# Kernel optimization log

Hardware: AMD Instinct MI355X
Metric: run time of the kernel (lower is better)

The kernel has to match this reference:

```python
import jax, jax.numpy as jnp
import numpy as np

N_NODES = 200000
N_EDGES = 3200000
NX = 8
NK = 2


def _l2norm(x, eps=1e-12):
    # F.normalize(x, p=2, dim=-1)
    n = jnp.linalg.norm(x, axis=-1, keepdims=True)
    return x / jnp.maximum(n, eps)


def _aniso_conv(x, src, dst, Kw, n_nodes):
    """For each kernel j: out_j[t] = sum_{e: dst[e]=t} Kw[j,e] * x[src[e]].
    Concatenate over kernels along the feature axis."""
    g = x[src]  # [E, d] gather
    def agg(w):  # w: [E]
        return jax.ops.segment_sum(w[:, None] * g, dst, num_segments=n_nodes)
    out = jax.vmap(agg)(Kw)  # [nk, N, d]
    return jnp.transpose(out, (1, 0, 2)).reshape(n_nodes, -1)  # [N, nk*d]


def setup_inputs() -> dict:
    key = jax.random.key(0)
    ks = jax.random.split(key, 8)
    x = jax.random.normal(ks[0], (N_NODES, NX), dtype=jnp.float32)
    src = jax.random.randint(ks[1], (N_EDGES,), 0, N_NODES, dtype=jnp.int64 if jax.config.jax_enable_x64 else jnp.int32)
    dst = jax.random.randint(ks[2], (N_EDGES,), 0, N_NODES, dtype=src.dtype)
    edge_index = jnp.stack([src, dst], axis=0)
    Kw = jax.random.normal(ks[3], (NK, N_EDGES), dtype=jnp.float32)
    d0, d1 = NX * NK, NX * NK * 2          # 16, 32
    d2 = d1 * NK                            # 64
    hidden, out_ch = 128, 64
    W0 = jax.random.normal(ks[4], (d0, d1), dtype=jnp.float32) / np.sqrt(d0)
    b0 = jnp.zeros((d1,), dtype=jnp.float32)
    W1 = jax.random.normal(ks[5], (d2, hidden), dtype=jnp.float32) / np.sqrt(d2)
    b1 = jnp.zeros((hidden,), dtype=jnp.float32)
    W2 = jax.random.normal(ks[6], (hidden, out_ch), dtype=jnp.float32) / np.sqrt(hidden)
    b2 = jnp.zeros((out_ch,), dtype=jnp.float32)
    return {"x": x, "edge_index": edge_index, "Kw": Kw,
            "W0": W0, "b0": b0, "W1": W1, "b1": b1, "W2": W2, "b2": b2}


def reference(x, edge_index, Kw, W0, b0, W1, b1, W2, b2):
    src, dst = edge_index[0], edge_index[1]
    n = x.shape[0]
    # layer 0: AnisoConv -> single-linear MLP -> L2 normalize
    h = _aniso_conv(x, src, dst, Kw, n)      # [N, 16]
    h = h @ W0 + b0                           # [N, 32]
    h = _l2norm(h)
    # layer 1: AnisoConv -> 2-layer MLP (ReLU between) -> L2 normalize
    h = _aniso_conv(h, src, dst, Kw, n)      # [N, 64]
    h = jax.nn.relu(h @ W1 + b1)             # [N, 128]
    h = h @ W2 + b2                           # [N, 64]
    h = _l2norm(h)
    return h
```

## Files before the change

### kernel.cpp

```cpp
#include <hip/hip_runtime.h>

#define NN 200000
#define NE 3200000
#define NB_SCAN 782
#define NBUCK 196
#define BSHIFT 10
#define BMASK 1023
#define SRCMASK 0x3FFFFu
#define NBLK_A 1024
#define EPB (NE / NBLK_A)
#define NPASS 13
#define EMAX 18
#define NT_MLP1 12500

using bf16x8 = __attribute__((ext_vector_type(8))) short;
using f32x4  = __attribute__((ext_vector_type(4))) float;

__device__ __forceinline__ float bflo(unsigned u) { return __uint_as_float(u << 16); }
__device__ __forceinline__ float bfhi(unsigned u) { return __uint_as_float(u & 0xffff0000u); }
__device__ __forceinline__ unsigned short f2bfu(float f) {
  unsigned u = __float_as_uint(f);
  return (unsigned short)((u + 0x7fffu + ((u >> 16) & 1u)) >> 16);
}
__device__ __forceinline__ unsigned pack2(float a, float b) {
  return (unsigned)f2bfu(a) | ((unsigned)f2bfu(b) << 16);
}

__device__ __forceinline__ void acc_edge(uint2 e, uint4 u, float* g0, float* g1) {
  float k0 = bflo(e.y), k1 = bfhi(e.y);
  float v0 = bflo(u.x), v1 = bfhi(u.x);
  float v2 = bflo(u.y), v3 = bfhi(u.y);
  float v4 = bflo(u.z), v5 = bfhi(u.z);
  float v6 = bflo(u.w), v7 = bfhi(u.w);
  g0[0] += k0 * v0; g0[1] += k0 * v1; g0[2] += k0 * v2; g0[3] += k0 * v3;
  g0[4] += k0 * v4; g0[5] += k0 * v5; g0[6] += k0 * v6; g0[7] += k0 * v7;
  g1[0] += k1 * v0; g1[1] += k1 * v1; g1[2] += k1 * v2; g1[3] += k1 * v3;
  g1[4] += k1 * v4; g1[5] += k1 * v5; g1[6] += k1 * v6; g1[7] += k1 * v7;
}


__global__ __launch_bounds__(256) void bhist_kernel(const int* __restrict__ dst,
                                                    int* __restrict__ bhT) {
  __shared__ int h[NBUCK];
  for (int k = threadIdx.x; k < NBUCK; k += 256) h[k] = 0;
  __syncthreads();
  int base = blockIdx.x * EPB;
  for (int i = threadIdx.x; i < EPB; i += 256)
    atomicAdd(&h[dst[base + i] >> BSHIFT], 1);
  __syncthreads();
  for (int k = threadIdx.x; k < NBUCK; k += 256)
    bhT[k * NBLK_A + blockIdx.x] = h[k];
}

__global__ __launch_bounds__(NBLK_A) void bscan_kernel(int* __restrict__ bhT,
                                                       int* __restrict__ btot) {
  __shared__ int s[NBLK_A];
  int b = blockIdx.x;
  int v = bhT[b * NBLK_A + threadIdx.x];
  s[threadIdx.x] = v;
  __syncthreads();
#pragma unroll
  for (int off = 1; off < NBLK_A; off <<= 1) {
    int t = (threadIdx.x >= off) ? s[threadIdx.x - off] : 0;
    __syncthreads();
    s[threadIdx.x] += t;
    __syncthreads();
  }
  bhT[b * NBLK_A + threadIdx.x] = s[threadIdx.x] - v;
  if (threadIdx.x == NBLK_A - 1) btot[b] = s[NBLK_A - 1];
}

__global__ __launch_bounds__(256) void bbase_kernel(const int* __restrict__ btot,
                                                    int* __restrict__ bbase) {
  __shared__ int s[256];
  int v = (threadIdx.x < NBUCK) ? btot[threadIdx.x] : 0;
  s[threadIdx.x] = v;
  __syncthreads();
#pragma unroll
  for (int off = 1; off < 256; off <<= 1) {
    int t = (threadIdx.x >= off) ? s[threadIdx.x - off] : 0;
    __syncthreads();
    s[threadIdx.x] += t;
    __syncthreads();
  }
  if (threadIdx.x < NBUCK) bbase[threadIdx.x] = s[threadIdx.x] - v;
  if (threadIdx.x == NBUCK - 1) bbase[NBUCK] = s[threadIdx.x];
}

__global__ __launch_bounds__(256) void bplace_kernel(
    const int* __restrict__ src, const int* __restrict__ dst,
    const float* __restrict__ kw, const int* __restrict__ bhT,
    const int* __restrict__ bbase, uint2* __restrict__ bsorted) {
  __shared__ int cur[NBUCK];
  for (int k = threadIdx.x; k < NBUCK; k += 256)
    cur[k] = bbase[k] + bhT[k * NBLK_A + blockIdx.x];
  __syncthreads();
  int base = blockIdx.x * EPB;
  for (int i = threadIdx.x; i < EPB; i += 256) {
    int e = base + i;
    int d = dst[e];
    int p = atomicAdd(&cur[d >> BSHIFT], 1);
    uint2 u;
    u.x = (unsigned)src[e] | ((unsigned)(d & BMASK) << 18);
    u.y = pack2(kw[e], kw[NE + e]);
    bsorted[p] = u;
  }
}


__global__ __launch_bounds__(1024) void nsort_kernel(
    const uint2* __restrict__ bsorted, const int* __restrict__ bbase,
    int* __restrict__ cnt, int* __restrict__ offs, uint2* __restrict__ sedge) {
  __shared__ int h[1024];
  __shared__ int cur[1024];
  int tid = threadIdx.x, b = blockIdx.x;
  h[tid] = 0;
  __syncthreads();
  int r0 = bbase[b], r1 = bbase[b + 1];
  int i0 = r0 + tid;

  uint2 e[EMAX];
#pragma unroll
  for (int j = 0; j < EMAX; ++j) {
    int i = i0 + j * 1024;
    if (i < r1) {
      e[j] = bsorted[i];
      atomicAdd(&h[e[j].x >> 18], 1);
    }
  }
  for (int i = i0 + EMAX * 1024; i < r1; i += 1024)
    atomicAdd(&h[bsorted[i].x >> 18], 1);
  __syncthreads();

  int v = h[tid];
  cur[tid] = v;
  __syncthreads();
  for (int off = 1; off < 1024; off <<= 1) {
    int t = (tid >= off) ? cur[tid - off] : 0;
    __syncthreads();
    cur[tid] += t;
    __syncthreads();
  }
  int excl = r0 + cur[tid] - v;
  int node = b * 1024 + tid;
  if (node < NN) { cnt[node] = v; offs[node] = excl; }
  __syncthreads();
  cur[tid] = excl;
  __syncthreads();

  for (int p = 0; p < NPASS; ++p) {
#pragma unroll
    for (int j = 0; j < EMAX; ++j) {
      int i = i0 + j * 1024;
      if (i < r1) {
        unsigned srcv = e[j].x & SRCMASK;
        if ((int)(srcv >> 14) == p) {
          int pos = atomicAdd(&cur[e[j].x >> 18], 1);
          uint2 w; w.x = srcv; w.y = e[j].y;
          sedge[pos] = w;
        }
      }
    }
    __syncthreads();
  }
  for (int i = i0 + EMAX * 1024; i < r1; i += 1024) {
    uint2 u = bsorted[i];
    int pos = atomicAdd(&cur[u.x >> 18], 1);
    u.x &= SRCMASK;
    sedge[pos] = u;
  }
}


__global__ __launch_bounds__(256) void xcvt_kernel(const float* __restrict__ x,
                                                   unsigned short* __restrict__ xbf) {
  int i = blockIdx.x * 256 + threadIdx.x;
  if (i >= NN) return;
  const float4* xp = reinterpret_cast<const float4*>(x + (size_t)i * 8);
  float4 a = xp[0], b = xp[1];
  uint4 u;
  u.x = pack2(a.x, a.y); u.y = pack2(a.z, a.w);
  u.z = pack2(b.x, b.y); u.w = pack2(b.z, b.w);
  *reinterpret_cast<uint4*>(xbf + (size_t)i * 8) = u;
}


__global__ __launch_bounds__(256) void fused0_kernel(
    const unsigned short* __restrict__ xbf, const int* __restrict__ offs,
    const int* __restrict__ cnt, const uint2* __restrict__ sedge,
    const float* __restrict__ W0, const float* __restrict__ b0,
    unsigned short* __restrict__ h1bf) {
  __shared__ float w0t[32][16];
  __shared__ float b0s[32];
  int tid = threadIdx.x;
  for (int i = tid; i < 16 * 32; i += 256) {
    int k = i >> 5, j = i & 31;
    w0t[j][k] = W0[i];
  }
  if (tid < 32) b0s[tid] = b0[tid];
  __syncthreads();

  int node = blockIdx.x * 256 + tid;
  if (node >= NN) return;

  int start = offs[node];
  int deg = cnt[node];
  float ha[8], hb[8];
#pragma unroll
  for (int k = 0; k < 8; ++k) { ha[k] = 0.f; hb[k] = 0.f; }

  int i = 0;
  for (; i + 4 <= deg; i += 4) {
    uint2 ee[4];
    uint4 uu[4];
#pragma unroll
    for (int j = 0; j < 4; ++j) ee[j] = sedge[start + i + j];
#pragma unroll
    for (int j = 0; j < 4; ++j)
      uu[j] = *reinterpret_cast<const uint4*>(xbf + (size_t)ee[j].x * 8);
#pragma unroll
    for (int j = 0; j < 4; ++j) acc_edge(ee[j], uu[j], ha, hb);
  }
  for (; i < deg; ++i) {
    uint2 e = sedge[start + i];
    uint4 u = *reinterpret_cast<const uint4*>(xbf + (size_t)e.x * 8);
    acc_edge(e, u, ha, hb);
  }

  float o[32];
  float ss = 0.f;
#pragma unroll
  for (int j = 0; j < 32; ++j) {
    float acc = b0s[j];
#pragma unroll
    for (int k = 0; k < 8; ++k) acc += ha[k] * w0t[j][k];
#pragma unroll
    for (int k = 0; k < 8; ++k) acc += hb[k] * w0t[j][8 + k];
    o[j] = acc;
    ss += acc * acc;
  }
  float inv = 1.f / fmaxf(sqrtf(ss), 1e-12f);
  uint4* op = reinterpret_cast<uint4*>(h1bf + (size_t)node * 32);
#pragma unroll
  for (int c = 0; c < 4; ++c) {
    uint4 u;
    u.x = pack2(o[c * 8 + 0] * inv, o[c * 8 + 1] * inv);
    u.y = pack2(o[c * 8 + 2] * inv, o[c * 8 + 3] * inv);
    u.z = pack2(o[c * 8 + 4] * inv, o[c * 8 + 5] * inv);
    u.w = pack2(o[c * 8 + 6] * inv, o[c * 8 + 7] * inv);
    op[c] = u;
  }
}


__global__ __launch_bounds__(256) void gather1_kernel(
    const unsigned short* __restrict__ h1bf, const int* __restrict__ offs,
    const int* __restrict__ cnt, const uint2* __restrict__ sedge,
    unsigned short* __restrict__ gbf) {
  int idx = blockIdx.x * 256 + threadIdx.x;
  int node = idx >> 2, q = idx & 3;
  int start = offs[node];
  int deg = cnt[node];

  float g0[8], g1[8];
#pragma unroll
  for (int k = 0; k < 8; ++k) { g0[k] = 0.f; g1[k] = 0.f; }

  int i = 0;
  for (; i + 8 <= deg; i += 8) {
    uint2 ee[8];
    uint4 uu[8];
#pragma unroll
    for (int j = 0; j < 8; ++j) ee[j] = sedge[start + i + j];
#pragma unroll
    for (int j = 0; j < 8; ++j)
      uu[j] = *reinterpret_cast<const uint4*>(h1bf + (size_t)ee[j].x * 32 + q * 8);
#pragma unroll
    for (int j = 0; j < 8; ++j) acc_edge(ee[j], uu[j], g0, g1);
  }
  for (; i + 4 <= deg; i += 4) {
    uint2 ee[4];
    uint4 uu[4];
#pragma unroll
    for (int j = 0; j < 4; ++j) ee[j] = sedge[start + i + j];
#pragma unroll
    for (int j = 0; j < 4; ++j)
      uu[j] = *reinterpret_cast<const uint4*>(h1bf + (size_t)ee[j].x * 32 + q * 8);
#pragma unroll
    for (int j = 0; j < 4; ++j) acc_edge(ee[j], uu[j], g0, g1);
  }
  for (; i < deg; ++i) {
    uint2 e = sedge[start + i];
    uint4 u = *reinterpret_cast<const uint4*>(h1bf + (size_t)e.x * 32 + q * 8);
    acc_edge(e, u, g0, g1);
  }

  uint4 s0, s1;
  s0.x = pack2(g0[0], g0[1]); s0.y = pack2(g0[2], g0[3]);
  s0.z = pack2(g0[4], g0[5]); s0.w = pack2(g0[6], g0[7]);
  s1.x = pack2(g1[0], g1[1]); s1.y = pack2(g1[2], g1[3]);
  s1.z = pack2(g1[4], g1[5]); s1.w = pack2(g1[6], g1[7]);
  *reinterpret_cast<uint4*>(gbf + (size_t)node * 64 + q * 8) = s0;
  *reinterpret_cast<uint4*>(gbf + (size_t)node * 64 + 32 + q * 8) = s1;
}


__global__ __launch_bounds__(256) void mlp1_kernel(
    const unsigned short* __restrict__ gbf,
    const float* __restrict__ W1, const float* __restrict__ b1,
    const float* __restrict__ W2, const float* __restrict__ b2,
    float* __restrict__ out) {
  __shared__ __align__(16) short hlds[4][16][136];
  int tid = threadIdx.x;
  int wave = tid >> 6, lane = tid & 63;
  int lg = lane >> 4;
  int lr = lane & 15;

  bf16x8 w1f[8][2];
#pragma unroll
  for (int n = 0; n < 8; ++n)
#pragma unroll
    for (int ks = 0; ks < 2; ++ks) {
      bf16x8 f;
#pragma unroll
      for (int i = 0; i < 8; ++i)
        f[i] = (short)f2bfu(W1[(size_t)(ks * 32 + lg * 8 + i) * 128 + n * 16 + lr]);
      w1f[n][ks] = f;
    }
  bf16x8 w2f[4][4];
#pragma unroll
  for (int n2 = 0; n2 < 4; ++n2)
#pragma unroll
    for (int ks = 0; ks < 4; ++ks) {
      bf16x8 f;
#pragma unroll
      for (int i = 0; i < 8; ++i)
        f[i] = (short)f2bfu(W2[(size_t)(ks * 32 + lg * 8 + i) * 64 + n2 * 16 + lr]);
      w2f[n2][ks] = f;
    }
  float b1v[8], b2v[4];
#pragma unroll
  for (int n = 0; n < 8; ++n) b1v[n] = b1[n * 16 + lr];
#pragma unroll
  for (int n2 = 0; n2 < 4; ++n2) b2v[n2] = b2[n2 * 16 + lr];

  for (int tile = blockIdx.x * 4 + wave; tile < NT_MLP1; tile += gridDim.x * 4) {
    int base = tile * 16;
    const bf16x8* grow = reinterpret_cast<const bf16x8*>(gbf + (size_t)(base + lr) * 64);
    bf16x8 a1_0 = grow[lg];
    bf16x8 a1_1 = grow[4 + lg];

#pragma unroll
    for (int n = 0; n < 8; ++n) {
      f32x4 acc = {0.f, 0.f, 0.f, 0.f};
      acc = __builtin_amdgcn_mfma_f32_16x16x32_bf16(a1_0, w1f[n][0], acc, 0, 0, 0);
      acc = __builtin_amdgcn_mfma_f32_16x16x32_bf16(a1_1, w1f[n][1], acc, 0, 0, 0);
#pragma unroll
      for (int q = 0; q < 4; ++q) {
        float v = fmaxf(acc[q] + b1v[n], 0.f);
        hlds[wave][lg * 4 + q][n * 16 + lr] = (short)f2bfu(v);
      }
    }

    bf16x8 a2[4];
#pragma unroll
    for (int ks = 0; ks < 4; ++ks)
      a2[ks] = *reinterpret_cast<const bf16x8*>(&hlds[wave][lr][ks * 32 + lg * 8]);
    f32x4 acc2[4];
#pragma unroll
    for (int n2 = 0; n2 < 4; ++n2) {
      f32x4 a = {0.f, 0.f, 0.f, 0.f};
#pragma unroll
      for (int ks = 0; ks < 4; ++ks)
        a = __builtin_amdgcn_mfma_f32_16x16x32_bf16(a2[ks], w2f[n2][ks], a, 0, 0, 0);
      acc2[n2] = a;
    }

#pragma unroll
    for (int q = 0; q < 4; ++q) {
      float s = 0.f;
#pragma unroll
      for (int n2 = 0; n2 < 4; ++n2) {
        float v = acc2[n2][q] + b2v[n2];
        s += v * v;
      }
      s += __shfl_xor(s, 1); s += __shfl_xor(s, 2);
      s += __shfl_xor(s, 4); s += __shfl_xor(s, 8);
      float inv = 1.f / fmaxf(sqrtf(s), 1e-12f);
      size_t rowoff = (size_t)(base + lg * 4 + q) * 64 + lr;
#pragma unroll
      for (int n2 = 0; n2 < 4; ++n2)
        out[rowoff + n2 * 16] = (acc2[n2][q] + b2v[n2]) * inv;
    }
  }
}


extern "C" void kernel_launch(void* const* d_in, const int* in_sizes, int n_in,
                              void* d_out, int out_size, void* d_ws, size_t ws_size,
                              hipStream_t stream) {
  const float* x  = (const float*)d_in[0];
  const int* ei   = (const int*)d_in[1];
  const float* kw = (const float*)d_in[2];
  const float* W0 = (const float*)d_in[3];
  const float* b0 = (const float*)d_in[4];
  const float* W1 = (const float*)d_in[5];
  const float* b1 = (const float*)d_in[6];
  const float* W2 = (const float*)d_in[7];
  const float* b2 = (const float*)d_in[8];
  float* out = (float*)d_out;

  const int* src = ei;
  const int* dst = ei + NE;

  char* p = (char*)d_ws;
  uint2* bsorted = (uint2*)p;                p += (size_t)NE * 8;
  uint2* sedge   = (uint2*)p;                p += (size_t)NE * 8;
  unsigned short* h1bf = (unsigned short*)p; p += (size_t)NN * 32 * 2;
  unsigned short* xbf  = (unsigned short*)p; p += (size_t)NN * 8 * 2;
  int* bhT   = (int*)p;                      p += (size_t)NBUCK * NBLK_A * 4;
  int* btot  = (int*)p;                      p += (size_t)NBUCK * 4;
  int* bbase = (int*)p;                      p += (size_t)(NBUCK + 1) * 4;
  int* cnt   = (int*)p;                      p += (size_t)NN * 4;
  int* offs  = (int*)p;                      p += (size_t)NN * 4;
  unsigned short* gbf = (unsigned short*)bsorted;

  xcvt_kernel<<<NB_SCAN, 256, 0, stream>>>(x, xbf);

  bhist_kernel<<<NBLK_A, 256, 0, stream>>>(dst, bhT);
  bscan_kernel<<<NBUCK, NBLK_A, 0, stream>>>(bhT, btot);
  bbase_kernel<<<1, 256, 0, stream>>>(btot, bbase);
  bplace_kernel<<<NBLK_A, 256, 0, stream>>>(src, dst, kw, bhT, bbase, bsorted);

  nsort_kernel<<<NBUCK, 1024, 0, stream>>>(bsorted, bbase, cnt, offs, sedge);

  fused0_kernel<<<NB_SCAN, 256, 0, stream>>>(xbf, offs, cnt, sedge, W0, b0, h1bf);
  gather1_kernel<<<(4 * NN) / 256, 256, 0, stream>>>(h1bf, offs, cnt, sedge, gbf);
  mlp1_kernel<<<768, 256, 0, stream>>>(gbf, W1, b1, W2, b2, out);
}
```

Measured before the change: 215.9 us.

## Stage bucket placement in LDS for coalesced global scatter

The bucket-placement kernel now sorts each block's edges locally in shared memory: it builds a per-block bucket histogram, scans it, places edges into an LDS staging buffer, then writes them out contiguously per bucket. This replaces the scattered per-edge global writes with mostly contiguous runs, aiming to coalesce the bucketed output stores. The block count is halved so each block handles more edges, which makes the runs longer but lowers parallelism and uses about 56KB of LDS per block, which limits occupancy.

```diff
diff --git a/kernel.cpp b/kernel.cpp
--- a/kernel.cpp
+++ b/kernel.cpp
@@ -7,7 +7,7 @@
 #define BSHIFT 10
 #define BMASK 1023
 #define SRCMASK 0x3FFFFu
-#define NBLK_A 1024
+#define NBLK_A 512
 #define EPB (NE / NBLK_A)
 #define NPASS 13
 #define EMAX 18
@@ -91,19 +91,52 @@
     const int* __restrict__ src, const int* __restrict__ dst,
     const float* __restrict__ kw, const int* __restrict__ bhT,
     const int* __restrict__ bbase, uint2* __restrict__ bsorted) {
-  __shared__ int cur[NBUCK];
-  for (int k = threadIdx.x; k < NBUCK; k += 256)
-    cur[k] = bbase[k] + bhT[k * NBLK_A + blockIdx.x];
-  __syncthreads();
-  int base = blockIdx.x * EPB;
-  for (int i = threadIdx.x; i < EPB; i += 256) {
+  __shared__ uint2 stage[EPB];
+  __shared__ unsigned char stageK[EPB];
+  __shared__ int h[256];
+  __shared__ int sc[256];
+  __shared__ int lof[256];
+  __shared__ int gof[256];
+  __shared__ int cur[256];
+  int tid = threadIdx.x, blk = blockIdx.x;
+  int base = blk * EPB;
+
+  h[tid] = 0;
+  __syncthreads();
+  for (int i = tid; i < EPB; i += 256)
+    atomicAdd(&h[dst[base + i] >> BSHIFT], 1);
+  __syncthreads();
+  int v = h[tid];
+  sc[tid] = v;
+  __syncthreads();
+#pragma unroll
+  for (int off = 1; off < 256; off <<= 1) {
+    int t = (tid >= off) ? sc[tid - off] : 0;
+    __syncthreads();
+    sc[tid] += t;
+    __syncthreads();
+  }
+  int excl = sc[tid] - v;
+  lof[tid] = excl;
+  cur[tid] = excl;
+  if (tid < NBUCK)
+    gof[tid] = bbase[tid] + bhT[tid * NBLK_A + blk] - excl;
+  __syncthreads();
+  for (int i = tid; i < EPB; i += 256) {
     int e = base + i;
     int d = dst[e];
-    int p = atomicAdd(&cur[d >> BSHIFT], 1);
+    int k = d >> BSHIFT;
+    int p = atomicAdd(&cur[k], 1);
     uint2 u;
     u.x = (unsigned)src[e] | ((unsigned)(d & BMASK) << 18);
     u.y = pack2(kw[e], kw[NE + e]);
-    bsorted[p] = u;
+    stage[p] = u;
+    stageK[p] = (unsigned char)k;
+  }
+  __syncthreads();
+  for (int i = tid; i < EPB; i += 256) {
+    int k = stageK[i];
+    bsorted[gof[k] + i] = stage[i];
   }
 }
 
```

New measurement: 210.4 us. 2.5% less time.
